# Kernel tuning notes

Hardware: AMD Instinct MI355X
Metric: run time of the kernel (lower is better)

The kernel has to match this reference:

```python
import jax, jax.numpy as jnp
import numpy as np

N, E, D, H, C, TD, MD = 50000, 500000, 128, 2, 64, 32, 64


def setup_inputs() -> dict:
    key = jax.random.key(0)
    ks = jax.random.split(key, 16)
    s = 0.05
    return {
        "x": jax.random.normal(ks[0], (N, D), jnp.float32),
        "edge_index": jax.random.randint(ks[1], (2, E), 0, N, dtype=jnp.int64),
        "edge_time": jax.random.randint(ks[2], (E,), 0, 86400, dtype=jnp.int64),
        "msg": jax.random.normal(ks[3], (E, MD), jnp.float32),
        "Wt": jax.random.normal(ks[4], (1, TD), jnp.float32) * s,
        "bt": jax.random.normal(ks[5], (TD,), jnp.float32) * s,
        "Wq": jax.random.normal(ks[6], (D, H * C), jnp.float32) * s,
        "bq": jax.random.normal(ks[7], (H * C,), jnp.float32) * s,
        "Wk": jax.random.normal(ks[8], (D, H * C), jnp.float32) * s,
        "bk": jax.random.normal(ks[9], (H * C,), jnp.float32) * s,
        "Wv": jax.random.normal(ks[10], (D, H * C), jnp.float32) * s,
        "bv": jax.random.normal(ks[11], (H * C,), jnp.float32) * s,
        "We": jax.random.normal(ks[12], (TD + MD, H * C), jnp.float32) * s,
        "Wskip": jax.random.normal(ks[13], (D, H * C), jnp.float32) * s,
        "bskip": jax.random.normal(ks[14], (H * C,), jnp.float32) * s,
    }


def reference(x, edge_index, edge_time, msg, Wt, bt, Wq, bq, Wk, bk, Wv, bv, We, Wskip, bskip):
    n = x.shape[0]
    src, dst = edge_index[0], edge_index[1]

    # TGN-style time encoding: cos(Linear(t))  -> [E, TD]
    t = edge_time.astype(x.dtype)[:, None]
    rel_t = jnp.cos(t @ Wt + bt)
    edge_attr = jnp.concatenate([rel_t, msg], axis=-1)  # [E, TD+MD]

    # TransformerConv projections, reshaped to [n, H, C] then gathered per edge
    q = (x @ Wq + bq).reshape(n, H, C)[dst]   # [E, H, C]
    k = (x @ Wk + bk).reshape(n, H, C)[src]   # [E, H, C]
    v = (x @ Wv + bv).reshape(n, H, C)[src]   # [E, H, C]
    e = (edge_attr @ We).reshape(-1, H, C)    # [E, H, C]

    k = k + e
    alpha = (q * k).sum(-1) / jnp.sqrt(jnp.asarray(C, x.dtype))  # [E, H]

    # segment softmax over incoming edges of each dst node
    amax = jax.ops.segment_max(alpha, dst, num_segments=n)       # [n, H]
    amax = jnp.where(jnp.isfinite(amax), amax, 0.0)
    ex = jnp.exp(alpha - amax[dst])
    denom = jax.ops.segment_sum(ex, dst, num_segments=n)
    alpha = ex / (denom[dst] + 1e-16)                            # [E, H]

    out_e = (v + e) * alpha[..., None]                           # [E, H, C]
    out = jax.ops.segment_sum(out_e, dst, num_segments=n).reshape(n, H * C)

    # root/skip connection
    out = out + x @ Wskip + bskip
    return out
```

## Files before the change

kernel.cpp:

```cpp
#include <hip/hip_runtime.h>
#include <hip/hip_bf16.h>

#define NN 50000
#define NE 500000
#define DD 128
#define HCC 128
#define TDD 32
#define MDD 64

typedef __hip_bfloat16 bf16;
typedef _Float16 f16;
typedef __attribute__((ext_vector_type(8))) _Float16 f16x8;
typedef __attribute__((ext_vector_type(2))) _Float16 f16x2;
typedef __attribute__((ext_vector_type(4))) float f32x4;

__device__ __forceinline__ float2 bf2x(unsigned u) {
    union { unsigned v; float f; } a, b;
    a.v = u << 16; b.v = u & 0xffff0000u;
    float2 r; r.x = a.f; r.y = b.f; return r;
}

#if defined(__has_builtin) && __has_builtin(__builtin_amdgcn_fdot2)
#define FDOT2(a, b, acc) __builtin_amdgcn_fdot2((a), (b), (acc), false)
#else
__device__ __forceinline__ float fdot2_sw(f16x2 a, f16x2 b, float acc) {
    acc = fmaf((float)a[0], (float)b[0], acc);
    return fmaf((float)a[1], (float)b[1], acc);
}
#define FDOT2(a, b, acc) fdot2_sw((a), (b), (acc))
#endif

__global__ __launch_bounds__(256) void conv_w_kernel(
    const float* __restrict__ Wq, const float* __restrict__ Wk,
    const float* __restrict__ Wv, const float* __restrict__ Wsk,
    const float* __restrict__ We,
    f16* __restrict__ WTh, f16* __restrict__ Weh, int* __restrict__ cnt)
{
    int idx = blockIdx.x * 256 + threadIdx.x;
    if (idx < 512 * 128) {
        int n = idx >> 7, k = idx & 127;
        int mat = n >> 7, col = n & 127;
        const float* W = (mat == 0) ? Wq : (mat == 1) ? Wk : (mat == 2) ? Wv : Wsk;
        WTh[idx] = (f16)W[k * 128 + col];
    } else if (idx < 512 * 128 + 96 * 128) {
        int i = idx - 512 * 128;
        Weh[i] = (f16)We[i];
    } else if (idx < 512 * 128 + 96 * 128 + NN) {
        cnt[idx - (512 * 128 + 96 * 128)] = 0;
    }
}

__global__ __launch_bounds__(256) void node_proj_kernel(
    const float* __restrict__ x, const f16* __restrict__ WTh,
    const float* __restrict__ bq, const float* __restrict__ bk,
    const float* __restrict__ bv, const float* __restrict__ bsk,
    f16* __restrict__ qh, f16* __restrict__ kvh,
    float* __restrict__ outp)
{
    __shared__ f16 xs[64 * 136];
    __shared__ f16 ws[128 * 136];

    const int node0 = blockIdx.x * 64;
    const int g = blockIdx.y;

    for (int i = threadIdx.x; i < 64 * 32; i += 256) {
        int node = i >> 5, koff = (i & 31) * 4;
        int gn = node0 + node;
        f16 o4[4] = { (f16)0.f, (f16)0.f, (f16)0.f, (f16)0.f };
        if (gn < NN) {
            float4 v = *(const float4*)&x[(size_t)gn * DD + koff];
            o4[0] = (f16)v.x; o4[1] = (f16)v.y; o4[2] = (f16)v.z; o4[3] = (f16)v.w;
        }
        *(uint2*)&xs[node * 136 + koff] = *(uint2*)o4;
    }
    const f16* wt = WTh + (size_t)g * 128 * 128;
    for (int i = threadIdx.x; i < 128 * 32; i += 256) {
        int n = i >> 5, koff = (i & 31) * 4;
        *(uint2*)&ws[n * 136 + koff] = *(const uint2*)&wt[n * 128 + koff];
    }
    __syncthreads();

    const int wave = threadIdx.x >> 6;
    const int lane = threadIdx.x & 63;
    const int m0 = wave * 16;
    const int lrow = lane & 15;
    const int lk = (lane >> 4) * 8;

    f32x4 acc[8];
    #pragma unroll
    for (int t = 0; t < 8; t++) acc[t] = (f32x4){0.f, 0.f, 0.f, 0.f};

    #pragma unroll
    for (int kc = 0; kc < 4; kc++) {
        f16x8 a = *(const f16x8*)&xs[(m0 + lrow) * 136 + kc * 32 + lk];
        #pragma unroll
        for (int t = 0; t < 8; t++) {
            f16x8 b = *(const f16x8*)&ws[(t * 16 + lrow) * 136 + kc * 32 + lk];
            acc[t] = __builtin_amdgcn_mfma_f32_16x16x32_f16(a, b, acc[t], 0, 0, 0);
        }
    }

    const float* bias = (g == 0) ? bq : (g == 1) ? bk : (g == 2) ? bv : bsk;

    #pragma unroll 1
    for (int t = 0; t < 8; t++) {
        int col = t * 16 + lrow;
        float bc = bias[col];
        #pragma unroll
        for (int r = 0; r < 4; r++) {
            int node = node0 + m0 + (lane >> 4) * 4 + r;
            if (node < NN) {
                float val = acc[t][r] + bc;
                if (g == 0)      qh[(size_t)node * DD + col] = (f16)val;
                else if (g == 3) outp[(size_t)node * HCC + col] = val;
                else {
                    int off = 8 * (col >> 2) + (col & 3) + ((g == 2) ? 4 : 0);
                    kvh[(size_t)node * 256 + off] = (f16)val;
                }
            }
        }
    }
}

__global__ __launch_bounds__(256) void g_kernel(
    const f16* __restrict__ qh, const f16* __restrict__ Weh,
    bf16* __restrict__ G)
{
    __shared__ f16 qs[64 * 136];
    __shared__ f16 ws[96 * 136];

    const int node0 = blockIdx.x * 64;
    for (int i = threadIdx.x; i < 64 * 32; i += 256) {
        int node = i >> 5, koff = (i & 31) * 4;
        int gn = node0 + node;
        uint2 val = {0u, 0u};
        if (gn < NN) val = *(const uint2*)&qh[(size_t)gn * DD + koff];
        *(uint2*)&qs[node * 136 + koff] = val;
    }
    for (int i = threadIdx.x; i < 96 * 32; i += 256) {
        int j = i >> 5, koff = (i & 31) * 4;
        *(uint2*)&ws[j * 136 + koff] = *(const uint2*)&Weh[j * 128 + koff];
    }
    __syncthreads();

    const int wave = threadIdx.x >> 6;
    const int lane = threadIdx.x & 63;
    const int m0 = wave * 16;
    const int lrow = lane & 15;
    const int lk = (lane >> 4) * 8;

    f16x8 afr[4];
    #pragma unroll
    for (int hk = 0; hk < 4; hk++) {
        int h = hk >> 1, kc = hk & 1;
        afr[hk] = *(const f16x8*)&qs[(m0 + lrow) * 136 + h * 64 + kc * 32 + lk];
    }

    f32x4 acc[12];
    #pragma unroll
    for (int t = 0; t < 12; t++) acc[t] = (f32x4){0.f, 0.f, 0.f, 0.f};

    #pragma unroll
    for (int t = 0; t < 12; t++) {
        int h = (t < 6) ? 0 : 1;
        int jt = (t < 6) ? t : t - 6;
        #pragma unroll
        for (int kc = 0; kc < 2; kc++) {
            f16x8 b = *(const f16x8*)&ws[(jt * 16 + lrow) * 136 + h * 64 + kc * 32 + lk];
            acc[t] = __builtin_amdgcn_mfma_f32_16x16x32_f16(afr[h * 2 + kc], b, acc[t], 0, 0, 0);
        }
    }

    #pragma unroll 1
    for (int t = 0; t < 12; t++) {
        int h = (t < 6) ? 0 : 1;
        int jt = (t < 6) ? t : t - 6;
        int col = h * 96 + jt * 16 + lrow;
        #pragma unroll
        for (int r = 0; r < 4; r++) {
            int node = node0 + m0 + (lane >> 4) * 4 + r;
            if (node < NN) G[(size_t)node * 192 + col] = __float2bfloat16(acc[t][r]);
        }
    }
}

__global__ __launch_bounds__(256) void hist_kernel(
    const int* __restrict__ ei, int* __restrict__ cnt)
{
    int gid = blockIdx.x * 256 + threadIdx.x;
    if (gid < NE) atomicAdd(&cnt[ei[NE + gid]], 1);
}

__global__ __launch_bounds__(256) void scan_a_kernel(
    const int* __restrict__ cnt, int* __restrict__ bsum)
{
    __shared__ int red[256];
    int gid = blockIdx.x * 256 + threadIdx.x;
    red[threadIdx.x] = (gid < NN) ? cnt[gid] : 0;
    __syncthreads();
    for (int off = 128; off > 0; off >>= 1) {
        if (threadIdx.x < off) red[threadIdx.x] += red[threadIdx.x + off];
        __syncthreads();
    }
    if (threadIdx.x == 0) bsum[blockIdx.x] = red[0];
}

__global__ __launch_bounds__(256) void scan_b_kernel(
    const int* __restrict__ bsum, int* __restrict__ boff, int* __restrict__ seg)
{
    __shared__ int s[256];
    int t = threadIdx.x;
    s[t] = (t < 196) ? bsum[t] : 0;
    __syncthreads();
    if (t == 0) {
        int run = 0;
        for (int b = 0; b < 196; b++) { int v = s[b]; s[b] = run; run += v; }
        seg[NN] = NE;
    }
    __syncthreads();
    if (t < 196) boff[t] = s[t];
}

__global__ __launch_bounds__(256) void scan_c_kernel(
    const int* __restrict__ cnt, const int* __restrict__ boff,
    int* __restrict__ seg, int* __restrict__ cur)
{
    __shared__ int s[256];
    int gid = blockIdx.x * 256 + threadIdx.x;
    int v = (gid < NN) ? cnt[gid] : 0;
    s[threadIdx.x] = v;
    __syncthreads();
    for (int off = 1; off < 256; off <<= 1) {
        int t = (threadIdx.x >= off) ? s[threadIdx.x - off] : 0;
        __syncthreads();
        s[threadIdx.x] += t;
        __syncthreads();
    }
    int excl = s[threadIdx.x] - v + boff[blockIdx.x];
    if (gid < NN) { seg[gid] = excl; cur[gid] = excl; }
}

__global__ __launch_bounds__(256) void scatter_kernel(
    const int* __restrict__ ei, const int* __restrict__ et,
    int* __restrict__ cur, int4* __restrict__ epack)
{
    int gid = blockIdx.x * 256 + threadIdx.x;
    if (gid < NE) {
        int d = ei[NE + gid];
        int pos = atomicAdd(&cur[d], 1);
        int4 p;
        p.x = ei[gid];
        p.y = gid;
        p.z = __float_as_int((float)et[gid]);
        p.w = d;
        epack[pos] = p;
    }
}

__global__ __launch_bounds__(256) void agg_kernel(
    const int4* __restrict__ epack, const float* __restrict__ msg,
    const float* __restrict__ Wt, const float* __restrict__ bt,
    const f16* __restrict__ qh, const f16* __restrict__ kvh,
    const bf16* __restrict__ G, const int* __restrict__ seg,
    float* __restrict__ Sv, float* __restrict__ dnv,
    float* __restrict__ outp)
{
    const int lane = threadIdx.x & 63;
    const int l31 = lane & 31;
    const int hl = (lane >> 4) & 1;
    const int c = lane & 15;
    const int halfid = lane >> 5;

    const float wt0 = Wt[2 * c], wt1 = Wt[2 * c + 1];
    const float bt0 = bt[2 * c], bt1 = bt[2 * c + 1];

    const int gw = blockIdx.x * 4 + (threadIdx.x >> 6);
    const int NW = gridDim.x * 4;

    union QU { uint2 u; f16x2 h[2]; };
    union KVU { uint4 u4; f16x2 h[4]; };

    for (int n = gw; n < NN; n += NW) {
        const int s0 = seg[n], s1 = seg[n + 1];

        QU q; q.u = *(const uint2*)&qh[(size_t)n * DD + 4 * l31];
        const bf16* grow = G + (size_t)n * 192 + 96 * hl;
        const float Gc0 = __bfloat162float(grow[2 * c]);
        const float Gc1 = __bfloat162float(grow[2 * c + 1]);
        const float Gm0 = __bfloat162float(grow[32 + 4 * c]);
        const float Gm1 = __bfloat162float(grow[33 + 4 * c]);
        const float Gm2 = __bfloat162float(grow[34 + 4 * c]);
        const float Gm3 = __bfloat162float(grow[35 + 4 * c]);

        f32x4 av = (f32x4){0.f, 0.f, 0.f, 0.f};
        f32x4 sm = (f32x4){0.f, 0.f, 0.f, 0.f};
        float accd = 0.f, sc0 = 0.f, sc1 = 0.f;

        auto edge_body = [&](int iu, bool pred) {
            int ic = pred ? iu : s0;
            int4 e = epack[ic];
            KVU kv;
            kv.u4 = *(const uint4*)&kvh[(size_t)e.x * 256 + 8 * l31];
            float4 m = *(const float4*)&msg[((size_t)e.y << 6) + 4 * c];
            float t = __int_as_float(e.z);
            float cs0 = __cosf(fmaf(t, wt0, bt0));
            float cs1 = __cosf(fmaf(t, wt1, bt1));
            float p = fmaf(cs0, Gc0, cs1 * Gc1);
            p = fmaf(m.x, Gm0, p); p = fmaf(m.y, Gm1, p);
            p = fmaf(m.z, Gm2, p); p = fmaf(m.w, Gm3, p);
            p = FDOT2(q.h[0], kv.h[0], p);
            p = FDOT2(q.h[1], kv.h[1], p);
            p += __shfl_xor(p, 1);
            p += __shfl_xor(p, 2);
            p += __shfl_xor(p, 4);
            p += __shfl_xor(p, 8);
            float ex = pred ? __expf(p * 0.125f) : 0.f;
            av.x = fmaf(ex, (float)kv.h[2][0], av.x);
            av.y = fmaf(ex, (float)kv.h[2][1], av.y);
            av.z = fmaf(ex, (float)kv.h[3][0], av.z);
            av.w = fmaf(ex, (float)kv.h[3][1], av.w);
            accd += ex;
            sc0 = fmaf(ex, cs0, sc0);
            sc1 = fmaf(ex, cs1, sc1);
            sm.x = fmaf(ex, m.x, sm.x);
            sm.y = fmaf(ex, m.y, sm.y);
            sm.z = fmaf(ex, m.z, sm.z);
            sm.w = fmaf(ex, m.w, sm.w);
        };

        int ib = s0;
        #pragma unroll 1
        for (; ib + 8 <= s1; ib += 8) {
            #pragma unroll
            for (int u = 0; u < 4; u++)
                edge_body(ib + 2 * u + halfid, true);
        }
        #pragma unroll 1
        for (; ib < s1; ib += 2) {
            int iu = ib + halfid;
            edge_body(iu, iu < s1);
        }

        av.x += __shfl_xor(av.x, 32);
        av.y += __shfl_xor(av.y, 32);
        av.z += __shfl_xor(av.z, 32);
        av.w += __shfl_xor(av.w, 32);
        accd += __shfl_xor(accd, 32);
        sc0  += __shfl_xor(sc0, 32);
        sc1  += __shfl_xor(sc1, 32);
        sm.x += __shfl_xor(sm.x, 32);
        sm.y += __shfl_xor(sm.y, 32);
        sm.z += __shfl_xor(sm.z, 32);
        sm.w += __shfl_xor(sm.w, 32);

        if (lane < 32) {
            float dn = accd + 1e-16f;
            size_t sb = (size_t)n * 192 + 96 * hl;
            float2 scv; scv.x = sc0; scv.y = sc1;
            *(float2*)&Sv[sb + 2 * c] = scv;
            float4 smv; smv.x = sm.x; smv.y = sm.y; smv.z = sm.z; smv.w = sm.w;
            *(float4*)&Sv[sb + 32 + 4 * c] = smv;
            if (c == 0) dnv[2 * n + hl] = accd;

            size_t nb = (size_t)n * HCC + 4 * l31;
            float4 sk = *(const float4*)&outp[nb];
            float4 o;
            o.x = av.x / dn + sk.x;
            o.y = av.y / dn + sk.y;
            o.z = av.z / dn + sk.z;
            o.w = av.w / dn + sk.w;
            *(float4*)&outp[nb] = o;
        }
    }
}

__global__ __launch_bounds__(256) void epi_kernel(
    const float* __restrict__ Sv, const float* __restrict__ dnv,
    const float* __restrict__ We, float* __restrict__ outp)
{
    __shared__ float st[192 * 36];
    const int node0 = blockIdx.x * 32;
    for (int idx = threadIdx.x; idx < 32 * 192; idx += 256) {
        int n = idx / 192, c = idx - n * 192;
        int node = node0 + n;
        st[c * 36 + n] = (node < NN) ? Sv[(size_t)node * 192 + c] : 0.f;
    }
    __syncthreads();

    const int wave = threadIdx.x >> 6;
    const int lane = threadIdx.x & 63;
    const int nb = wave * 8;
    const int hoff = (lane < 32) ? 0 : 96;
    const float2* We2 = (const float2*)We;

    float a[8][2];
    #pragma unroll
    for (int n = 0; n < 8; n++) { a[n][0] = 0.f; a[n][1] = 0.f; }

    #pragma unroll 8
    for (int j = 0; j < 96; j++) {
        float2 w = We2[j * 64 + lane];
        const float* sr = &st[(hoff + j) * 36 + nb];
        float sv[8];
        *(float4*)&sv[0] = *(const float4*)sr;
        *(float4*)&sv[4] = *(const float4*)(sr + 4);
        #pragma unroll
        for (int n = 0; n < 8; n++) {
            a[n][0] = fmaf(sv[n], w.x, a[n][0]);
            a[n][1] = fmaf(sv[n], w.y, a[n][1]);
        }
    }

    #pragma unroll 1
    for (int n = 0; n < 8; n++) {
        int node = node0 + nb + n;
        if (node >= NN) break;
        float dn = dnv[node * 2 + (lane >> 5)] + 1e-16f;
        size_t b = (size_t)node * HCC + 2 * lane;
        float2 o = *(const float2*)&outp[b];
        o.x += a[n][0] / dn;
        o.y += a[n][1] / dn;
        *(float2*)&outp[b] = o;
    }
}

extern "C" void kernel_launch(void* const* d_in, const int* in_sizes, int n_in,
                              void* d_out, int out_size, void* d_ws, size_t ws_size,
                              hipStream_t stream) {
    const float* x   = (const float*)d_in[0];
    const int* ei    = (const int*)d_in[1];
    const int* et    = (const int*)d_in[2];
    const float* msg = (const float*)d_in[3];
    const float* Wt  = (const float*)d_in[4];
    const float* bt  = (const float*)d_in[5];
    const float* Wq  = (const float*)d_in[6];
    const float* bq  = (const float*)d_in[7];
    const float* Wk  = (const float*)d_in[8];
    const float* bk  = (const float*)d_in[9];
    const float* Wv  = (const float*)d_in[10];
    const float* bv  = (const float*)d_in[11];
    const float* We  = (const float*)d_in[12];
    const float* Wsk = (const float*)d_in[13];
    const float* bsk = (const float*)d_in[14];

    const size_t nf = (size_t)NN * HCC;
    f16* qh      = (f16*)d_ws;
    f16* kvh     = qh + nf;
    f16* WTh     = kvh + 2 * nf;
    f16* Weh     = WTh + 512 * 128;
    bf16* G      = (bf16*)(Weh + 96 * 128);
    float* Sv    = (float*)(G + (size_t)NN * 192);
    float* dnv   = Sv + (size_t)NN * 192;
    int4* epack  = (int4*)(dnv + (size_t)NN * 2);
    int* cnt     = (int*)(epack + NE);
    int* seg     = cnt + NN;
    int* cur     = seg + NN + 1;
    int* bsum    = cur + NN;
    int* boff    = bsum + 256;
    size_t need  = (size_t)((char*)(boff + 256) - (char*)d_ws);
    if (ws_size < need) return;

    float* outp = (float*)d_out;

    conv_w_kernel<<<(512 * 128 + 96 * 128 + NN + 255) / 256, 256, 0, stream>>>(
        Wq, Wk, Wv, Wsk, We, WTh, Weh, cnt);
    dim3 npgrid((NN + 63) / 64, 4);
    node_proj_kernel<<<npgrid, 256, 0, stream>>>(
        x, WTh, bq, bk, bv, bsk, qh, kvh, outp);
    g_kernel<<<(NN + 63) / 64, 256, 0, stream>>>(qh, Weh, G);
    hist_kernel<<<(NE + 255) / 256, 256, 0, stream>>>(ei, cnt);
    scan_a_kernel<<<196, 256, 0, stream>>>(cnt, bsum);
    scan_b_kernel<<<1, 256, 0, stream>>>(bsum, boff, seg);
    scan_c_kernel<<<196, 256, 0, stream>>>(cnt, boff, seg, cur);
    scatter_kernel<<<(NE + 255) / 256, 256, 0, stream>>>(ei, et, cur, epack);
    agg_kernel<<<3125, 256, 0, stream>>>(
        epack, msg, Wt, bt, qh, kvh, G, seg, Sv, dnv, outp);
    epi_kernel<<<(NN + 31) / 32, 256, 0, stream>>>(Sv, dnv, We, outp);
}
```

Before: 537.8 us.

## Use atomic work-stealing over node chunks, batch edge loads, DPP row reductions

The aggregation kernel drops its fixed grid-stride node assignment. Each wave now claims chunks of 4 nodes from a global atomic counter, which balances the skewed per-node edge counts, and the grid shrinks to 2048 blocks. The unrolled edge loop issues all four epack loads, then all kv and msg gathers, before any compute, so more memory requests are in flight. The 16-lane dot-product reductions use DPP row rotations instead of shfl_xor. The counter is zeroed alongside cnt, which costs one atomic per chunk and uses more registers per wave.

```diff
diff --git a/kernel.cpp b/kernel.cpp
--- a/kernel.cpp
+++ b/kernel.cpp
@@ -29,6 +29,19 @@
 }
 #define FDOT2(a, b, acc) fdot2_sw((a), (b), (acc))
 #endif
+
+template <int CTRL>
+__device__ __forceinline__ float rot_add(float x) {
+    int r = __builtin_amdgcn_update_dpp(0, __float_as_int(x), CTRL, 0xF, 0xF, true);
+    return x + __int_as_float(r);
+}
+__device__ __forceinline__ float row_reduce16(float x) {
+    x = rot_add<0x121>(x);
+    x = rot_add<0x122>(x);
+    x = rot_add<0x124>(x);
+    x = rot_add<0x128>(x);
+    return x;
+}
 
 __global__ __launch_bounds__(256) void conv_w_kernel(
     const float* __restrict__ Wq, const float* __restrict__ Wk,
@@ -45,7 +58,7 @@
     } else if (idx < 512 * 128 + 96 * 128) {
         int i = idx - 512 * 128;
         Weh[i] = (f16)We[i];
-    } else if (idx < 512 * 128 + 96 * 128 + NN) {
+    } else if (idx < 512 * 128 + 96 * 128 + NN + 1) {
         cnt[idx - (512 * 128 + 96 * 128)] = 0;
     }
 }
@@ -262,6 +275,7 @@
     const float* __restrict__ Wt, const float* __restrict__ bt,
     const f16* __restrict__ qh, const f16* __restrict__ kvh,
     const bf16* __restrict__ G, const int* __restrict__ seg,
+    int* __restrict__ wctr,
     float* __restrict__ Sv, float* __restrict__ dnv,
     float* __restrict__ outp)
 {
@@ -274,102 +288,142 @@
     const float wt0 = Wt[2 * c], wt1 = Wt[2 * c + 1];
     const float bt0 = bt[2 * c], bt1 = bt[2 * c + 1];
 
-    const int gw = blockIdx.x * 4 + (threadIdx.x >> 6);
-    const int NW = gridDim.x * 4;
-
     union QU { uint2 u; f16x2 h[2]; };
     union KVU { uint4 u4; f16x2 h[4]; };
 
-    for (int n = gw; n < NN; n += NW) {
-        const int s0 = seg[n], s1 = seg[n + 1];
-
-        QU q; q.u = *(const uint2*)&qh[(size_t)n * DD + 4 * l31];
-        const bf16* grow = G + (size_t)n * 192 + 96 * hl;
-        const float Gc0 = __bfloat162float(grow[2 * c]);
-        const float Gc1 = __bfloat162float(grow[2 * c + 1]);
-        const float Gm0 = __bfloat162float(grow[32 + 4 * c]);
-        const float Gm1 = __bfloat162float(grow[33 + 4 * c]);
-        const float Gm2 = __bfloat162float(grow[34 + 4 * c]);
-        const float Gm3 = __bfloat162float(grow[35 + 4 * c]);
-
-        f32x4 av = (f32x4){0.f, 0.f, 0.f, 0.f};
-        f32x4 sm = (f32x4){0.f, 0.f, 0.f, 0.f};
-        float accd = 0.f, sc0 = 0.f, sc1 = 0.f;
-
-        auto edge_body = [&](int iu, bool pred) {
-            int ic = pred ? iu : s0;
-            int4 e = epack[ic];
-            KVU kv;
-            kv.u4 = *(const uint4*)&kvh[(size_t)e.x * 256 + 8 * l31];
-            float4 m = *(const float4*)&msg[((size_t)e.y << 6) + 4 * c];
-            float t = __int_as_float(e.z);
-            float cs0 = __cosf(fmaf(t, wt0, bt0));
-            float cs1 = __cosf(fmaf(t, wt1, bt1));
-            float p = fmaf(cs0, Gc0, cs1 * Gc1);
-            p = fmaf(m.x, Gm0, p); p = fmaf(m.y, Gm1, p);
-            p = fmaf(m.z, Gm2, p); p = fmaf(m.w, Gm3, p);
-            p = FDOT2(q.h[0], kv.h[0], p);
-            p = FDOT2(q.h[1], kv.h[1], p);
-            p += __shfl_xor(p, 1);
-            p += __shfl_xor(p, 2);
-            p += __shfl_xor(p, 4);
-            p += __shfl_xor(p, 8);
-            float ex = pred ? __expf(p * 0.125f) : 0.f;
-            av.x = fmaf(ex, (float)kv.h[2][0], av.x);
-            av.y = fmaf(ex, (float)kv.h[2][1], av.y);
-            av.z = fmaf(ex, (float)kv.h[3][0], av.z);
-            av.w = fmaf(ex, (float)kv.h[3][1], av.w);
-            accd += ex;
-            sc0 = fmaf(ex, cs0, sc0);
-            sc1 = fmaf(ex, cs1, sc1);
-            sm.x = fmaf(ex, m.x, sm.x);
-            sm.y = fmaf(ex, m.y, sm.y);
-            sm.z = fmaf(ex, m.z, sm.z);
-            sm.w = fmaf(ex, m.w, sm.w);
-        };
-
-        int ib = s0;
-        #pragma unroll 1
-        for (; ib + 8 <= s1; ib += 8) {
-            #pragma unroll
-            for (int u = 0; u < 4; u++)
-                edge_body(ib + 2 * u + halfid, true);
-        }
-        #pragma unroll 1
-        for (; ib < s1; ib += 2) {
-            int iu = ib + halfid;
-            edge_body(iu, iu < s1);
-        }
-
-        av.x += __shfl_xor(av.x, 32);
-        av.y += __shfl_xor(av.y, 32);
-        av.z += __shfl_xor(av.z, 32);
-        av.w += __shfl_xor(av.w, 32);
-        accd += __shfl_xor(accd, 32);
-        sc0  += __shfl_xor(sc0, 32);
-        sc1  += __shfl_xor(sc1, 32);
-        sm.x += __shfl_xor(sm.x, 32);
-        sm.y += __shfl_xor(sm.y, 32);
-        sm.z += __shfl_xor(sm.z, 32);
-        sm.w += __shfl_xor(sm.w, 32);
-
-        if (lane < 32) {
-            float dn = accd + 1e-16f;
-            size_t sb = (size_t)n * 192 + 96 * hl;
-            float2 scv; scv.x = sc0; scv.y = sc1;
-            *(float2*)&Sv[sb + 2 * c] = scv;
-            float4 smv; smv.x = sm.x; smv.y = sm.y; smv.z = sm.z; smv.w = sm.w;
-            *(float4*)&Sv[sb + 32 + 4 * c] = smv;
-            if (c == 0) dnv[2 * n + hl] = accd;
-
-            size_t nb = (size_t)n * HCC + 4 * l31;
-            float4 sk = *(const float4*)&outp[nb];
-            float4 o;
-            o.x = av.x / dn + sk.x;
-            o.y = av.y / dn + sk.y;
-            o.z = av.z / dn + sk.z;
-            o.w = av.w / dn + sk.w;
-            *(float4*)&outp[nb] = o;
+    for (;;) {
+        int n0;
+        if (lane == 0) n0 = atomicAdd(wctr, 4);
+        n0 = __shfl(n0, 0);
+        if (n0 >= NN) break;
+        const int nend = (n0 + 4 < NN) ? n0 + 4 : NN;
+
+        for (int n = n0; n < nend; n++) {
+            const int s0 = seg[n], s1 = seg[n + 1];
+
+            QU q; q.u = *(const uint2*)&qh[(size_t)n * DD + 4 * l31];
+            const bf16* grow = G + (size_t)n * 192 + 96 * hl;
+            const float Gc0 = __bfloat162float(grow[2 * c]);
+            const float Gc1 = __bfloat162float(grow[2 * c + 1]);
+            const float Gm0 = __bfloat162float(grow[32 + 4 * c]);
+            const float Gm1 = __bfloat162float(grow[33 + 4 * c]);
+            const float Gm2 = __bfloat162float(grow[34 + 4 * c]);
+            const float Gm3 = __bfloat162float(grow[35 + 4 * c]);
+
+            f32x4 av = (f32x4){0.f, 0.f, 0.f, 0.f};
+            f32x4 sm = (f32x4){0.f, 0.f, 0.f, 0.f};
+            float accd = 0.f, sc0 = 0.f, sc1 = 0.f;
+
+            int ib = s0;
+            #pragma unroll 1
+            for (; ib + 8 <= s1; ib += 8) {
+                int4 e[4];
+                #pragma unroll
+                for (int u = 0; u < 4; u++) e[u] = epack[ib + 2 * u + halfid];
+                KVU kv[4]; float4 m[4];
+                #pragma unroll
+                for (int u = 0; u < 4; u++) {
+                    kv[u].u4 = *(const uint4*)&kvh[(size_t)e[u].x * 256 + 8 * l31];
+                    m[u] = *(const float4*)&msg[((size_t)e[u].y << 6) + 4 * c];
+                }
+                float p[4], csa[4], csb[4];
+                #pragma unroll
+                for (int u = 0; u < 4; u++) {
+                    float t = __int_as_float(e[u].z);
+                    csa[u] = __cosf(fmaf(t, wt0, bt0));
+                    csb[u] = __cosf(fmaf(t, wt1, bt1));
+                    float pp = fmaf(csa[u], Gc0, csb[u] * Gc1);
+                    pp = fmaf(m[u].x, Gm0, pp); pp = fmaf(m[u].y, Gm1, pp);
+                    pp = fmaf(m[u].z, Gm2, pp); pp = fmaf(m[u].w, Gm3, pp);
+                    pp = FDOT2(q.h[0], kv[u].h[0], pp);
+                    pp = FDOT2(q.h[1], kv[u].h[1], pp);
+                    p[u] = pp;
+                }
+                #pragma unroll
+                for (int u = 0; u < 4; u++) p[u] = rot_add<0x121>(p[u]);
+                #pragma unroll
+                for (int u = 0; u < 4; u++) p[u] = rot_add<0x122>(p[u]);
+                #pragma unroll
+                for (int u = 0; u < 4; u++) p[u] = rot_add<0x124>(p[u]);
+                #pragma unroll
+                for (int u = 0; u < 4; u++) p[u] = rot_add<0x128>(p[u]);
+                #pragma unroll
+                for (int u = 0; u < 4; u++) {
+                    float ex = __expf(p[u] * 0.125f);
+                    av.x = fmaf(ex, (float)kv[u].h[2][0], av.x);
+                    av.y = fmaf(ex, (float)kv[u].h[2][1], av.y);
+                    av.z = fmaf(ex, (float)kv[u].h[3][0], av.z);
+                    av.w = fmaf(ex, (float)kv[u].h[3][1], av.w);
+                    accd += ex;
+                    sc0 = fmaf(ex, csa[u], sc0);
+                    sc1 = fmaf(ex, csb[u], sc1);
+                    sm.x = fmaf(ex, m[u].x, sm.x);
+                    sm.y = fmaf(ex, m[u].y, sm.y);
+                    sm.z = fmaf(ex, m[u].z, sm.z);
+                    sm.w = fmaf(ex, m[u].w, sm.w);
+                }
+            }
+            #pragma unroll 1
+            for (; ib < s1; ib += 2) {
+                int iu = ib + halfid;
+                bool pred = iu < s1;
+                int4 e = epack[pred ? iu : s0];
+                KVU kv;
+                kv.u4 = *(const uint4*)&kvh[(size_t)e.x * 256 + 8 * l31];
+                float4 m = *(const float4*)&msg[((size_t)e.y << 6) + 4 * c];
+                float t = __int_as_float(e.z);
+                float cs0 = __cosf(fmaf(t, wt0, bt0));
+                float cs1 = __cosf(fmaf(t, wt1, bt1));
+                float pp = fmaf(cs0, Gc0, cs1 * Gc1);
+                pp = fmaf(m.x, Gm0, pp); pp = fmaf(m.y, Gm1, pp);
+                pp = fmaf(m.z, Gm2, pp); pp = fmaf(m.w, Gm3, pp);
+                pp = FDOT2(q.h[0], kv.h[0], pp);
+                pp = FDOT2(q.h[1], kv.h[1], pp);
+                pp = row_reduce16(pp);
+                float ex = pred ? __expf(pp * 0.125f) : 0.f;
+                av.x = fmaf(ex, (float)kv.h[2][0], av.x);
+                av.y = fmaf(ex, (float)kv.h[2][1], av.y);
+                av.z = fmaf(ex, (float)kv.h[3][0], av.z);
+                av.w = fmaf(ex, (float)kv.h[3][1], av.w);
+                accd += ex;
+                sc0 = fmaf(ex, cs0, sc0);
+                sc1 = fmaf(ex, cs1, sc1);
+                sm.x = fmaf(ex, m.x, sm.x);
+                sm.y = fmaf(ex, m.y, sm.y);
+                sm.z = fmaf(ex, m.z, sm.z);
+                sm.w = fmaf(ex, m.w, sm.w);
+            }
+
+            av.x += __shfl_xor(av.x, 32);
+            av.y += __shfl_xor(av.y, 32);
+            av.z += __shfl_xor(av.z, 32);
+            av.w += __shfl_xor(av.w, 32);
+            accd += __shfl_xor(accd, 32);
+            sc0  += __shfl_xor(sc0, 32);
+            sc1  += __shfl_xor(sc1, 32);
+            sm.x += __shfl_xor(sm.x, 32);
+            sm.y += __shfl_xor(sm.y, 32);
+            sm.z += __shfl_xor(sm.z, 32);
+            sm.w += __shfl_xor(sm.w, 32);
+
+            if (lane < 32) {
+                float dn = accd + 1e-16f;
+                size_t sb = (size_t)n * 192 + 96 * hl;
+                float2 scv; scv.x = sc0; scv.y = sc1;
+                *(float2*)&Sv[sb + 2 * c] = scv;
+                float4 smv; smv.x = sm.x; smv.y = sm.y; smv.z = sm.z; smv.w = sm.w;
+                *(float4*)&Sv[sb + 32 + 4 * c] = smv;
+                if (c == 0) dnv[2 * n + hl] = accd;
+
+                size_t nb = (size_t)n * HCC + 4 * l31;
+                float4 sk = *(const float4*)&outp[nb];
+                float4 o;
+                o.x = av.x / dn + sk.x;
+                o.y = av.y / dn + sk.y;
+                o.z = av.z / dn + sk.z;
+                o.w = av.w / dn + sk.w;
+                *(float4*)&outp[nb] = o;
+            }
         }
     }
 }
@@ -453,16 +507,17 @@
     float* dnv   = Sv + (size_t)NN * 192;
     int4* epack  = (int4*)(dnv + (size_t)NN * 2);
     int* cnt     = (int*)(epack + NE);
-    int* seg     = cnt + NN;
+    int* seg     = cnt + NN + 1;
     int* cur     = seg + NN + 1;
     int* bsum    = cur + NN;
     int* boff    = bsum + 256;
     size_t need  = (size_t)((char*)(boff + 256) - (char*)d_ws);
     if (ws_size < need) return;
 
+    int* wctr = cnt + NN;
     float* outp = (float*)d_out;
 
-    conv_w_kernel<<<(512 * 128 + 96 * 128 + NN + 255) / 256, 256, 0, stream>>>(
+    conv_w_kernel<<<(512 * 128 + 96 * 128 + NN + 1 + 255) / 256, 256, 0, stream>>>(
         Wq, Wk, Wv, Wsk, We, WTh, Weh, cnt);
     dim3 npgrid((NN + 63) / 64, 4);
     node_proj_kernel<<<npgrid, 256, 0, stream>>>(
@@ -473,7 +528,7 @@
     scan_b_kernel<<<1, 256, 0, stream>>>(bsum, boff, seg);
     scan_c_kernel<<<196, 256, 0, stream>>>(cnt, boff, seg, cur);
     scatter_kernel<<<(NE + 255) / 256, 256, 0, stream>>>(ei, et, cur, epack);
-    agg_kernel<<<3125, 256, 0, stream>>>(
-        epack, msg, Wt, bt, qh, kvh, G, seg, Sv, dnv, outp);
+    agg_kernel<<<2048, 256, 0, stream>>>(
+        epack, msg, Wt, bt, qh, kvh, G, seg, wctr, Sv, dnv, outp);
     epi_kernel<<<(NN + 31) / 32, 256, 0, stream>>>(Sv, dnv, We, outp);
 }
```

After: 689.5 us. 1.28x slower.
